# Kernel tuning notes

Hardware: AMD Instinct MI355X
Metric: run time of the kernel (lower is better)

The kernel has to match this reference:

```python
import jax, jax.numpy as jnp
import numpy as np

HEADS = 16

def setup_inputs() -> dict:
    key = jax.random.key(0)
    k1, k2, k3 = jax.random.split(key, 3)
    B, S, D = 4, 2048, 1024
    x = jax.random.normal(k1, (B, S, D), dtype=jnp.float32)
    w_qkv = jax.random.normal(k2, (D, 3 * D), dtype=jnp.float32) * (D ** -0.5)
    w_out = jax.random.normal(k3, (D, D), dtype=jnp.float32) * (D ** -0.5)
    return {"x": x, "w_qkv": w_qkv, "w_out": w_out}

def reference(x, w_qkv, w_out):
    B, S, D = x.shape
    H = HEADS
    hd = D // H
    qkv = jnp.einsum("bsd,de->bse", x, w_qkv)  # [B,S,3D]
    q, k, v = jnp.split(qkv, 3, axis=-1)
    # [B,S,D] -> [B,H,S,hd]
    q = q.reshape(B, S, H, hd).transpose(0, 2, 1, 3)
    k = k.reshape(B, S, H, hd).transpose(0, 2, 1, 3)
    v = v.reshape(B, S, H, hd).transpose(0, 2, 1, 3)
    scores = jnp.einsum("bhqd,bhkd->bhqk", q, k) / jnp.sqrt(jnp.float32(hd))
    attn = jax.nn.softmax(scores, axis=-1)
    out = jnp.einsum("bhqk,bhkd->bhqd", attn, v)  # [B,H,S,hd]
    out = out.transpose(0, 2, 1, 3).reshape(B, S, D)
    return jnp.einsum("bsd,de->bse", out, w_out)
```

## Files before the change

### kernel.cpp

```cpp
#include <hip/hip_runtime.h>

typedef __bf16 bf16;
typedef __bf16 bfx8 __attribute__((ext_vector_type(8)));
typedef __bf16 bfx4 __attribute__((ext_vector_type(4)));
typedef float f32x4 __attribute__((ext_vector_type(4)));

#define MFMA_BF16 __builtin_amdgcn_mfma_f32_16x16x32_bf16

static constexpr int Bq = 4, Sq = 2048, Dq = 1024, Hq = 16, HDq = 64;
static constexpr int Mq = Bq * Sq;
static constexpr int D3 = 3 * Dq;
static constexpr float L2E = 1.4426950408889634f;
static constexpr float QSC = 0.125f * L2E;

typedef const __attribute__((address_space(1))) void* gas1;
typedef __attribute__((address_space(3))) void* las3;

__device__ __forceinline__ void gload_lds16(const bf16* g, bf16* l) {
    __builtin_amdgcn_global_load_lds((gas1)g, (las3)l, 16, 0, 0);
}

__device__ __forceinline__ float fast_exp2(float x) {
    return __builtin_amdgcn_exp2f(x);
}

__global__ __launch_bounds__(256) void cast_f32_bf16(const float* __restrict__ in,
                                                     bf16* __restrict__ out, int n) {
    int i = (blockIdx.x * 256 + threadIdx.x) * 4;
    if (i + 3 < n) {
        float4 v = *(const float4*)(in + i);
        bfx4 r;
        r[0] = (bf16)v.x; r[1] = (bf16)v.y; r[2] = (bf16)v.z; r[3] = (bf16)v.w;
        *(bfx4*)(out + i) = r;
    }
}

__global__ __launch_bounds__(256) void transpose_cast(const float* __restrict__ in,
                                                      bf16* __restrict__ out, int R, int C) {
    __shared__ float tile[32][33];
    int tx = threadIdx.x, ty = threadIdx.y;
    int c0 = blockIdx.x * 32, r0 = blockIdx.y * 32;
    for (int j = 0; j < 32; j += 8)
        tile[ty + j][tx] = in[(size_t)(r0 + ty + j) * C + c0 + tx];
    __syncthreads();
    for (int j = 0; j < 32; j += 8)
        out[(size_t)(c0 + ty + j) * R + r0 + tx] = (bf16)tile[tx][ty + j];
}

__global__ __launch_bounds__(256) void vtrans(const bf16* __restrict__ qkv,
                                              bf16* __restrict__ Vt) {
    __shared__ bf16 tile[32][33];
    int tx = threadIdx.x, ty = threadIdx.y;
    int c0 = blockIdx.x * 32;
    int s0 = blockIdx.y * 32;
    int b = blockIdx.z;
    for (int j = 0; j < 32; j += 8)
        tile[ty + j][tx] = qkv[(size_t)(b * Sq + s0 + ty + j) * D3 + 2 * Dq + c0 + tx];
    __syncthreads();
    for (int j = 0; j < 32; j += 8)
        Vt[((size_t)b * Dq + c0 + ty + j) * Sq + s0 + tx] = tile[tx][ty + j];
}

template <bool OUT_F32, bool QSCALE>
__global__ __launch_bounds__(256) void gemm_bt(const bf16* __restrict__ A,
                                               const bf16* __restrict__ Bt,
                                               void* __restrict__ Cout,
                                               int M, int N, int K) {
    __shared__ bf16 As[128 * 64];
    __shared__ bf16 Bs[128 * 64];
    int m0 = blockIdx.y * 128;
    int n0 = blockIdx.x * 128;
    int tid = threadIdx.x;
    int lane = tid & 63, wave = tid >> 6;
    int quad = lane >> 4, l16 = lane & 15;
    int wr = wave >> 1, wc = wave & 1;
    int sw = l16 & 7;

    f32x4 acc[4][4] = {};

    for (int k0 = 0; k0 < K; k0 += 64) {
        __syncthreads();
        #pragma unroll
        for (int i = 0; i < 4; i++) {
            int c = i * 256 + tid;
            int row = c >> 3;
            int ch = (c & 7) ^ (row & 7);
            gload_lds16(A + (size_t)(m0 + row) * K + k0 + ch * 8, As + c * 8);
            gload_lds16(Bt + (size_t)(n0 + row) * K + k0 + ch * 8, Bs + c * 8);
        }
        __syncthreads();
        #pragma unroll
        for (int s = 0; s < 2; s++) {
            bfx8 af[4], bfr[4];
            #pragma unroll
            for (int i = 0; i < 4; i++)
                af[i] = *(const bfx8*)(As + (wr * 64 + i * 16 + l16) * 64 +
                                       ((s * 4 + quad) ^ sw) * 8);
            #pragma unroll
            for (int j = 0; j < 4; j++)
                bfr[j] = *(const bfx8*)(Bs + (wc * 64 + j * 16 + l16) * 64 +
                                        ((s * 4 + quad) ^ sw) * 8);
            #pragma unroll
            for (int i = 0; i < 4; i++)
                #pragma unroll
                for (int j = 0; j < 4; j++)
                    acc[i][j] = MFMA_BF16(af[i], bfr[j], acc[i][j], 0, 0, 0);
        }
    }

    #pragma unroll
    for (int i = 0; i < 4; i++)
        #pragma unroll
        for (int j = 0; j < 4; j++) {
            int col = n0 + wc * 64 + j * 16 + l16;
            float scale = (QSCALE && col < Dq) ? QSC : 1.0f;
            #pragma unroll
            for (int r = 0; r < 4; r++) {
                int row = m0 + wr * 64 + i * 16 + quad * 4 + r;
                if (OUT_F32)
                    ((float*)Cout)[(size_t)row * N + col] = acc[i][j][r];
                else
                    ((bf16*)Cout)[(size_t)row * N + col] = (bf16)(acc[i][j][r] * scale);
            }
        }
}

__global__ __launch_bounds__(256, 4) void attn_kernel(const bf16* __restrict__ qkv,
                                                      const bf16* __restrict__ Vt,
                                                      bf16* __restrict__ out) {
    __shared__ bf16 Ks[2][64 * 64];
    __shared__ bf16 Vs[2][64 * 64];
    __shared__ bf16 Ps[4][32 * 32];

    int bid = blockIdx.x;
    int qc = (bid >> 3) & 15;
    int head = ((bid >> 7) << 3) | (bid & 7);
    int h = head & 15, b = head >> 4;
    int tid = threadIdx.x;
    int lane = tid & 63, wave = tid >> 6;
    int quad = lane >> 4, l16 = lane & 15;
    int sw = l16 & 7;
    int sw4 = l16 & 3;

    size_t base = (size_t)b * Sq * D3;
    const bf16* Kbase = qkv + base + Dq + h * HDq;
    const bf16* Vbase = Vt + ((size_t)b * Dq + h * HDq) * Sq;
    int q0 = qc * 128 + wave * 32;

    bfx8 qf[2][2];
    #pragma unroll
    for (int qt = 0; qt < 2; qt++)
        #pragma unroll
        for (int s = 0; s < 2; s++)
            qf[qt][s] = *(const bfx8*)(qkv + base + (size_t)(q0 + qt * 16 + l16) * D3 +
                                       h * HDq + s * 32 + quad * 8);

    bfx8 ones;
    #pragma unroll
    for (int j = 0; j < 8; j++) ones[j] = (bf16)1.0f;

    f32x4 oacc[2][4] = {};
    f32x4 lacc[2] = {};

    int c0 = tid, c1 = tid + 256;
    int r0 = c0 >> 3, ch0 = (c0 & 7) ^ (r0 & 7);
    int r1 = c1 >> 3, ch1 = (c1 & 7) ^ (r1 & 7);

    gload_lds16(Kbase + (size_t)r0 * D3 + ch0 * 8, Ks[0] + c0 * 8);
    gload_lds16(Vbase + (size_t)r0 * Sq + ch0 * 8, Vs[0] + c0 * 8);
    gload_lds16(Kbase + (size_t)r1 * D3 + ch1 * 8, Ks[0] + c1 * 8);
    gload_lds16(Vbase + (size_t)r1 * Sq + ch1 * 8, Vs[0] + c1 * 8);

    for (int i = 0; i < 32; i++) {
        int cur = i & 1;
        __syncthreads();
        if (i + 1 < 32) {
            int k0 = (i + 1) * 64;
            bf16* kd = Ks[cur ^ 1];
            bf16* vd = Vs[cur ^ 1];
            gload_lds16(Kbase + (size_t)(k0 + r0) * D3 + ch0 * 8, kd + c0 * 8);
            gload_lds16(Vbase + (size_t)r0 * Sq + k0 + ch0 * 8, vd + c0 * 8);
            gload_lds16(Kbase + (size_t)(k0 + r1) * D3 + ch1 * 8, kd + c1 * 8);
            gload_lds16(Vbase + (size_t)r1 * Sq + k0 + ch1 * 8, vd + c1 * 8);
        }
        const bf16* K_ = Ks[cur];
        const bf16* V_ = Vs[cur];

        #pragma unroll
        for (int hf = 0; hf < 2; hf++) {
            bfx8 kf[2][2];
            #pragma unroll
            for (int tp = 0; tp < 2; tp++) {
                int krow = ((2 * hf + tp) * 16 + l16) * 64;
                kf[tp][0] = *(const bfx8*)(K_ + krow + (quad ^ sw) * 8);
                kf[tp][1] = *(const bfx8*)(K_ + krow + ((4 + quad) ^ sw) * 8);
            }

            #pragma unroll
            for (int qt = 0; qt < 2; qt++) {
                f32x4 s[2] = {};
                #pragma unroll
                for (int tp = 0; tp < 2; tp++) {
                    s[tp] = MFMA_BF16(kf[tp][0], qf[qt][0], s[tp], 0, 0, 0);
                    s[tp] = MFMA_BF16(kf[tp][1], qf[qt][1], s[tp], 0, 0, 0);
                }
                #pragma unroll
                for (int tp = 0; tp < 2; tp++) {
                    bfx4 pk;
                    #pragma unroll
                    for (int r = 0; r < 4; r++)
                        pk[r] = (bf16)fast_exp2(s[tp][r]);
                    int slot = (2 * tp + (quad >> 1)) ^ sw4;
                    *(bfx4*)(&Ps[wave][(qt * 16 + l16) * 32 + slot * 8 + (quad & 1) * 4]) = pk;
                }
            }

            bfx8 pf[2];
            #pragma unroll
            for (int qt = 0; qt < 2; qt++) {
                pf[qt] = *(const bfx8*)(&Ps[wave][(qt * 16 + l16) * 32 + (quad ^ sw4) * 8]);
                lacc[qt] = MFMA_BF16(pf[qt], ones, lacc[qt], 0, 0, 0);
            }

            #pragma unroll
            for (int nt = 0; nt < 4; nt++) {
                bfx8 vf = *(const bfx8*)(V_ + (nt * 16 + l16) * 64 +
                                         ((hf * 4 + quad) ^ sw) * 8);
                #pragma unroll
                for (int qt = 0; qt < 2; qt++)
                    oacc[qt][nt] = MFMA_BF16(pf[qt], vf, oacc[qt][nt], 0, 0, 0);
            }
        }
    }

    #pragma unroll
    for (int qt = 0; qt < 2; qt++)
        #pragma unroll
        for (int r = 0; r < 4; r++) {
            int row = q0 + qt * 16 + quad * 4 + r;
            float inv = 1.0f / lacc[qt][r];
            #pragma unroll
            for (int nt = 0; nt < 4; nt++)
                out[((size_t)b * Sq + row) * Dq + h * HDq + nt * 16 + l16] =
                    (bf16)(oacc[qt][nt][r] * inv);
        }
}

extern "C" void kernel_launch(void* const* d_in, const int* in_sizes, int n_in,
                              void* d_out, int out_size, void* d_ws, size_t ws_size,
                              hipStream_t stream) {
    const float* x     = (const float*)d_in[0];
    const float* w_qkv = (const float*)d_in[1];
    const float* w_out = (const float*)d_in[2];
    float* out = (float*)d_out;

    char* ws = (char*)d_ws;
    bf16* x_bf   = (bf16*)ws;
    bf16* wqkvT  = (bf16*)(ws + 16777216);
    bf16* woutT  = (bf16*)(ws + 16777216 + 6291456);
    bf16* qkv    = (bf16*)(ws + 16777216 + 6291456 + 2097152);
    bf16* attn   = (bf16*)(ws + 16777216 + 6291456 + 2097152 + 50331648);
    bf16* Vt     = x_bf;

    cast_f32_bf16<<<(Mq * Dq) / 4 / 256, 256, 0, stream>>>(x, x_bf, Mq * Dq);
    dim3 tb(32, 8);
    transpose_cast<<<dim3(D3 / 32, Dq / 32), tb, 0, stream>>>(w_qkv, wqkvT, Dq, D3);
    transpose_cast<<<dim3(Dq / 32, Dq / 32), tb, 0, stream>>>(w_out, woutT, Dq, Dq);

    gemm_bt<false, true><<<dim3(D3 / 128, Mq / 128), 256, 0, stream>>>(x_bf, wqkvT, qkv, Mq, D3, Dq);

    vtrans<<<dim3(Dq / 32, Sq / 32, Bq), tb, 0, stream>>>(qkv, Vt);

    attn_kernel<<<1024, 256, 0, stream>>>(qkv, Vt, attn);

    gemm_bt<true, false><<<dim3(Dq / 128, Mq / 128), 256, 0, stream>>>(attn, woutT, out, Mq, Dq, Dq);
}
```

Before: 268.8 us.

## Fuse V transpose into QKV GEMM epilogue and keep P in registers

The QKV GEMM epilogue now writes V directly in a transposed, permuted layout into a separate buffer, and Q/K go to a narrower 2D-wide buffer, which removes the standalone vtrans kernel and its round trip through memory. The V sequence index is permuted so that the attention kernel can feed exp'd score registers straight into the PV MFMA as the A operand, dropping the per-wave LDS staging of P and the reads that followed it. The risk is scattered 8-byte stores in the GEMM epilogue for the V columns, and a correctness dependence on the permutation matching the MFMA register layout.

```diff
diff --git a/kernel.cpp b/kernel.cpp
--- a/kernel.cpp
+++ b/kernel.cpp
@@ -10,6 +10,7 @@
 static constexpr int Bq = 4, Sq = 2048, Dq = 1024, Hq = 16, HDq = 64;
 static constexpr int Mq = Bq * Sq;
 static constexpr int D3 = 3 * Dq;
+static constexpr int NQK = 2 * Dq;
 static constexpr float L2E = 1.4426950408889634f;
 static constexpr float QSC = 0.125f * L2E;
 
@@ -47,24 +48,11 @@
         out[(size_t)(c0 + ty + j) * R + r0 + tx] = (bf16)tile[tx][ty + j];
 }
 
-__global__ __launch_bounds__(256) void vtrans(const bf16* __restrict__ qkv,
-                                              bf16* __restrict__ Vt) {
-    __shared__ bf16 tile[32][33];
-    int tx = threadIdx.x, ty = threadIdx.y;
-    int c0 = blockIdx.x * 32;
-    int s0 = blockIdx.y * 32;
-    int b = blockIdx.z;
-    for (int j = 0; j < 32; j += 8)
-        tile[ty + j][tx] = qkv[(size_t)(b * Sq + s0 + ty + j) * D3 + 2 * Dq + c0 + tx];
-    __syncthreads();
-    for (int j = 0; j < 32; j += 8)
-        Vt[((size_t)b * Dq + c0 + ty + j) * Sq + s0 + tx] = tile[tx][ty + j];
-}
-
-template <bool OUT_F32, bool QSCALE>
+template <bool OUT_F32, bool QSCALE, bool VSPLIT>
 __global__ __launch_bounds__(256) void gemm_bt(const bf16* __restrict__ A,
                                                const bf16* __restrict__ Bt,
                                                void* __restrict__ Cout,
+                                               bf16* __restrict__ Vout,
                                                int M, int N, int K) {
     __shared__ bf16 As[128 * 64];
     __shared__ bf16 Bs[128 * 64];
@@ -113,14 +101,28 @@
         #pragma unroll
         for (int j = 0; j < 4; j++) {
             int col = n0 + wc * 64 + j * 16 + l16;
-            float scale = (QSCALE && col < Dq) ? QSC : 1.0f;
-            #pragma unroll
-            for (int r = 0; r < 4; r++) {
-                int row = m0 + wr * 64 + i * 16 + quad * 4 + r;
-                if (OUT_F32)
-                    ((float*)Cout)[(size_t)row * N + col] = acc[i][j][r];
-                else
-                    ((bf16*)Cout)[(size_t)row * N + col] = (bf16)(acc[i][j][r] * scale);
+            if (VSPLIT && col >= NQK) {
+                int d = col - NQK;
+                int row0 = m0 + wr * 64 + i * 16 + quad * 4;
+                int b = row0 >> 11, s0 = row0 & (Sq - 1);
+                int w = s0 & 63;
+                int sp = (s0 & ~63) | (((w >> 5) * 4 + ((w >> 2) & 3)) * 8) |
+                         (((w >> 4) & 1) * 4);
+                bfx4 pv;
+                #pragma unroll
+                for (int r = 0; r < 4; r++) pv[r] = (bf16)acc[i][j][r];
+                *(bfx4*)(Vout + ((size_t)b * Dq + d) * Sq + sp) = pv;
+            } else {
+                int cstride = VSPLIT ? NQK : N;
+                float scale = (QSCALE && col < Dq) ? QSC : 1.0f;
+                #pragma unroll
+                for (int r = 0; r < 4; r++) {
+                    int row = m0 + wr * 64 + i * 16 + quad * 4 + r;
+                    if (OUT_F32)
+                        ((float*)Cout)[(size_t)row * cstride + col] = acc[i][j][r];
+                    else
+                        ((bf16*)Cout)[(size_t)row * cstride + col] = (bf16)(acc[i][j][r] * scale);
+                }
             }
         }
 }
@@ -130,7 +132,6 @@
                                                       bf16* __restrict__ out) {
     __shared__ bf16 Ks[2][64 * 64];
     __shared__ bf16 Vs[2][64 * 64];
-    __shared__ bf16 Ps[4][32 * 32];
 
     int bid = blockIdx.x;
     int qc = (bid >> 3) & 15;
@@ -140,9 +141,8 @@
     int lane = tid & 63, wave = tid >> 6;
     int quad = lane >> 4, l16 = lane & 15;
     int sw = l16 & 7;
-    int sw4 = l16 & 3;
-
-    size_t base = (size_t)b * Sq * D3;
+
+    size_t base = (size_t)b * Sq * NQK;
     const bf16* Kbase = qkv + base + Dq + h * HDq;
     const bf16* Vbase = Vt + ((size_t)b * Dq + h * HDq) * Sq;
     int q0 = qc * 128 + wave * 32;
@@ -152,7 +152,7 @@
     for (int qt = 0; qt < 2; qt++)
         #pragma unroll
         for (int s = 0; s < 2; s++)
-            qf[qt][s] = *(const bfx8*)(qkv + base + (size_t)(q0 + qt * 16 + l16) * D3 +
+            qf[qt][s] = *(const bfx8*)(qkv + base + (size_t)(q0 + qt * 16 + l16) * NQK +
                                        h * HDq + s * 32 + quad * 8);
 
     bfx8 ones;
@@ -166,9 +166,9 @@
     int r0 = c0 >> 3, ch0 = (c0 & 7) ^ (r0 & 7);
     int r1 = c1 >> 3, ch1 = (c1 & 7) ^ (r1 & 7);
 
-    gload_lds16(Kbase + (size_t)r0 * D3 + ch0 * 8, Ks[0] + c0 * 8);
+    gload_lds16(Kbase + (size_t)r0 * NQK + ch0 * 8, Ks[0] + c0 * 8);
     gload_lds16(Vbase + (size_t)r0 * Sq + ch0 * 8, Vs[0] + c0 * 8);
-    gload_lds16(Kbase + (size_t)r1 * D3 + ch1 * 8, Ks[0] + c1 * 8);
+    gload_lds16(Kbase + (size_t)r1 * NQK + ch1 * 8, Ks[0] + c1 * 8);
     gload_lds16(Vbase + (size_t)r1 * Sq + ch1 * 8, Vs[0] + c1 * 8);
 
     for (int i = 0; i < 32; i++) {
@@ -178,9 +178,9 @@
             int k0 = (i + 1) * 64;
             bf16* kd = Ks[cur ^ 1];
             bf16* vd = Vs[cur ^ 1];
-            gload_lds16(Kbase + (size_t)(k0 + r0) * D3 + ch0 * 8, kd + c0 * 8);
+            gload_lds16(Kbase + (size_t)(k0 + r0) * NQK + ch0 * 8, kd + c0 * 8);
             gload_lds16(Vbase + (size_t)r0 * Sq + k0 + ch0 * 8, vd + c0 * 8);
-            gload_lds16(Kbase + (size_t)(k0 + r1) * D3 + ch1 * 8, kd + c1 * 8);
+            gload_lds16(Kbase + (size_t)(k0 + r1) * NQK + ch1 * 8, kd + c1 * 8);
             gload_lds16(Vbase + (size_t)r1 * Sq + k0 + ch1 * 8, vd + c1 * 8);
         }
         const bf16* K_ = Ks[cur];
@@ -196,29 +196,21 @@
                 kf[tp][1] = *(const bfx8*)(K_ + krow + ((4 + quad) ^ sw) * 8);
             }
 
+            bfx8 pf[2];
             #pragma unroll
             for (int qt = 0; qt < 2; qt++) {
-                f32x4 s[2] = {};
-                #pragma unroll
-                for (int tp = 0; tp < 2; tp++) {
-                    s[tp] = MFMA_BF16(kf[tp][0], qf[qt][0], s[tp], 0, 0, 0);
-                    s[tp] = MFMA_BF16(kf[tp][1], qf[qt][1], s[tp], 0, 0, 0);
+                f32x4 s0 = {}, s1 = {};
+                s0 = MFMA_BF16(kf[0][0], qf[qt][0], s0, 0, 0, 0);
+                s0 = MFMA_BF16(kf[0][1], qf[qt][1], s0, 0, 0, 0);
+                s1 = MFMA_BF16(kf[1][0], qf[qt][0], s1, 0, 0, 0);
+                s1 = MFMA_BF16(kf[1][1], qf[qt][1], s1, 0, 0, 0);
+                bfx8 p;
+                #pragma unroll
+                for (int r = 0; r < 4; r++) {
+                    p[r]     = (bf16)fast_exp2(s0[r]);
+                    p[4 + r] = (bf16)fast_exp2(s1[r]);
                 }
-                #pragma unroll
-                for (int tp = 0; tp < 2; tp++) {
-                    bfx4 pk;
-                    #pragma unroll
-                    for (int r = 0; r < 4; r++)
-                        pk[r] = (bf16)fast_exp2(s[tp][r]);
-                    int slot = (2 * tp + (quad >> 1)) ^ sw4;
-                    *(bfx4*)(&Ps[wave][(qt * 16 + l16) * 32 + slot * 8 + (quad & 1) * 4]) = pk;
-                }
-            }
-
-            bfx8 pf[2];
-            #pragma unroll
-            for (int qt = 0; qt < 2; qt++) {
-                pf[qt] = *(const bfx8*)(&Ps[wave][(qt * 16 + l16) * 32 + (quad ^ sw4) * 8]);
+                pf[qt] = p;
                 lacc[qt] = MFMA_BF16(pf[qt], ones, lacc[qt], 0, 0, 0);
             }
 
@@ -258,20 +250,20 @@
     bf16* x_bf   = (bf16*)ws;
     bf16* wqkvT  = (bf16*)(ws + 16777216);
     bf16* woutT  = (bf16*)(ws + 16777216 + 6291456);
-    bf16* qkv    = (bf16*)(ws + 16777216 + 6291456 + 2097152);
-    bf16* attn   = (bf16*)(ws + 16777216 + 6291456 + 2097152 + 50331648);
-    bf16* Vt     = x_bf;
+    bf16* qkv2   = (bf16*)(ws + 25165824);
+    bf16* Vt     = (bf16*)(ws + 25165824 + 33554432);
+    bf16* attn   = x_bf;
 
     cast_f32_bf16<<<(Mq * Dq) / 4 / 256, 256, 0, stream>>>(x, x_bf, Mq * Dq);
     dim3 tb(32, 8);
     transpose_cast<<<dim3(D3 / 32, Dq / 32), tb, 0, stream>>>(w_qkv, wqkvT, Dq, D3);
     transpose_cast<<<dim3(Dq / 32, Dq / 32), tb, 0, stream>>>(w_out, woutT, Dq, Dq);
 
-    gemm_bt<false, true><<<dim3(D3 / 128, Mq / 128), 256, 0, stream>>>(x_bf, wqkvT, qkv, Mq, D3, Dq);
-
-    vtrans<<<dim3(Dq / 32, Sq / 32, Bq), tb, 0, stream>>>(qkv, Vt);
-
-    attn_kernel<<<1024, 256, 0, stream>>>(qkv, Vt, attn);
-
-    gemm_bt<true, false><<<dim3(Dq / 128, Mq / 128), 256, 0, stream>>>(attn, woutT, out, Mq, Dq, Dq);
-}
+    gemm_bt<false, true, true><<<dim3(D3 / 128, Mq / 128), 256, 0, stream>>>(
+        x_bf, wqkvT, qkv2, Vt, Mq, D3, Dq);
+
+    attn_kernel<<<1024, 256, 0, stream>>>(qkv2, Vt, attn);
+
+    gemm_bt<true, false, false><<<dim3(Dq / 128, Mq / 128), 256, 0, stream>>>(
+        attn, woutT, out, nullptr, Mq, Dq, Dq);
+}
```

Result: faster. 257.8 us (-4.1%).

## Keep softmax probabilities in registers via permuted V layout and swizzle GEMM blocks

Applied to the files above, without the earlier changes.

The attention kernel no longer round-trips exp'd scores through LDS. It packs the two MFMA score tiles directly into the B-operand register fragment. To make this valid, the V transpose kernel permutes key positions within each 32-column block so that V's k-ordering matches the register layout of P. It also adds s_setprio around MFMA groups and an XCD-style block index swizzle in the GEMM to improve L2 locality. The risk is correctness coupling between the vtrans permutation and the fragment layout.

```diff
diff --git a/kernel.cpp b/kernel.cpp
--- a/kernel.cpp
+++ b/kernel.cpp
@@ -56,9 +56,10 @@
     int b = blockIdx.z;
     for (int j = 0; j < 32; j += 8)
         tile[ty + j][tx] = qkv[(size_t)(b * Sq + s0 + ty + j) * D3 + 2 * Dq + c0 + tx];
+    int src = 16 * ((tx >> 2) & 1) + 4 * (tx >> 3) + (tx & 3);
     __syncthreads();
     for (int j = 0; j < 32; j += 8)
-        Vt[((size_t)b * Dq + c0 + ty + j) * Sq + s0 + tx] = tile[tx][ty + j];
+        Vt[((size_t)b * Dq + c0 + ty + j) * Sq + s0 + tx] = tile[src][ty + j];
 }
 
 template <bool OUT_F32, bool QSCALE>
@@ -68,8 +69,11 @@
                                                int M, int N, int K) {
     __shared__ bf16 As[128 * 64];
     __shared__ bf16 Bs[128 * 64];
-    int m0 = blockIdx.y * 128;
-    int n0 = blockIdx.x * 128;
+    int nwg = gridDim.x * gridDim.y;
+    int lin = blockIdx.y * gridDim.x + blockIdx.x;
+    int swzb = (lin & 7) * (nwg >> 3) + (lin >> 3);
+    int m0 = (swzb / gridDim.x) * 128;
+    int n0 = (swzb % gridDim.x) * 128;
     int tid = threadIdx.x;
     int lane = tid & 63, wave = tid >> 6;
     int quad = lane >> 4, l16 = lane & 15;
@@ -130,7 +134,6 @@
                                                       bf16* __restrict__ out) {
     __shared__ bf16 Ks[2][64 * 64];
     __shared__ bf16 Vs[2][64 * 64];
-    __shared__ bf16 Ps[4][32 * 32];
 
     int bid = blockIdx.x;
     int qc = (bid >> 3) & 15;
@@ -140,7 +143,6 @@
     int lane = tid & 63, wave = tid >> 6;
     int quad = lane >> 4, l16 = lane & 15;
     int sw = l16 & 7;
-    int sw4 = l16 & 3;
 
     size_t base = (size_t)b * Sq * D3;
     const bf16* Kbase = qkv + base + Dq + h * HDq;
@@ -196,40 +198,36 @@
                 kf[tp][1] = *(const bfx8*)(K_ + krow + ((4 + quad) ^ sw) * 8);
             }
 
+            bfx8 pf[2];
             #pragma unroll
             for (int qt = 0; qt < 2; qt++) {
-                f32x4 s[2] = {};
+                f32x4 s0 = {}, s1 = {};
+                __builtin_amdgcn_s_setprio(1);
+                s0 = MFMA_BF16(kf[0][0], qf[qt][0], s0, 0, 0, 0);
+                s0 = MFMA_BF16(kf[0][1], qf[qt][1], s0, 0, 0, 0);
+                s1 = MFMA_BF16(kf[1][0], qf[qt][0], s1, 0, 0, 0);
+                s1 = MFMA_BF16(kf[1][1], qf[qt][1], s1, 0, 0, 0);
+                __builtin_amdgcn_s_setprio(0);
+                bfx8 p;
                 #pragma unroll
-                for (int tp = 0; tp < 2; tp++) {
-                    s[tp] = MFMA_BF16(kf[tp][0], qf[qt][0], s[tp], 0, 0, 0);
-                    s[tp] = MFMA_BF16(kf[tp][1], qf[qt][1], s[tp], 0, 0, 0);
+                for (int r = 0; r < 4; r++) {
+                    p[r]     = (bf16)fast_exp2(s0[r]);
+                    p[4 + r] = (bf16)fast_exp2(s1[r]);
                 }
-                #pragma unroll
-                for (int tp = 0; tp < 2; tp++) {
-                    bfx4 pk;
-                    #pragma unroll
-                    for (int r = 0; r < 4; r++)
-                        pk[r] = (bf16)fast_exp2(s[tp][r]);
-                    int slot = (2 * tp + (quad >> 1)) ^ sw4;
-                    *(bfx4*)(&Ps[wave][(qt * 16 + l16) * 32 + slot * 8 + (quad & 1) * 4]) = pk;
-                }
-            }
-
-            bfx8 pf[2];
-            #pragma unroll
-            for (int qt = 0; qt < 2; qt++) {
-                pf[qt] = *(const bfx8*)(&Ps[wave][(qt * 16 + l16) * 32 + (quad ^ sw4) * 8]);
-                lacc[qt] = MFMA_BF16(pf[qt], ones, lacc[qt], 0, 0, 0);
-            }
-
+                pf[qt] = p;
+            }
+
+            __builtin_amdgcn_s_setprio(1);
+            lacc[0] = MFMA_BF16(pf[0], ones, lacc[0], 0, 0, 0);
+            lacc[1] = MFMA_BF16(pf[1], ones, lacc[1], 0, 0, 0);
             #pragma unroll
             for (int nt = 0; nt < 4; nt++) {
                 bfx8 vf = *(const bfx8*)(V_ + (nt * 16 + l16) * 64 +
                                          ((hf * 4 + quad) ^ sw) * 8);
-                #pragma unroll
-                for (int qt = 0; qt < 2; qt++)
-                    oacc[qt][nt] = MFMA_BF16(pf[qt], vf, oacc[qt][nt], 0, 0, 0);
-            }
+                oacc[0][nt] = MFMA_BF16(pf[0], vf, oacc[0][nt], 0, 0, 0);
+                oacc[1][nt] = MFMA_BF16(pf[1], vf, oacc[1][nt], 0, 0, 0);
+            }
+            __builtin_amdgcn_s_setprio(0);
         }
     }
 
```

Result: no change. 264.1 us (-1.7%).
